# Kernel optimization log

Measured on AMD Instinct MI355X. Metric: run time of the kernel, lower is better.

The kernel has to match this reference:

```python
import jax, jax.numpy as jnp
import numpy as np

N_QUBITS = 4
DEPTH = 2
INV_SQRT2 = 0.7071067811865476

# --- batched real-valued 4-qubit state-vector simulator -------------------
# State: (N, 2, 2, 2, 2). All gates used (H, RY, CNOT) are real matrices, so
# the whole simulation runs in real float32 arithmetic.

def _apply_h(state, q):
    s = jnp.moveaxis(state, 1 + q, 1)
    a0, a1 = s[:, 0], s[:, 1]
    s = jnp.stack([(a0 + a1) * INV_SQRT2, (a0 - a1) * INV_SQRT2], axis=1)
    return jnp.moveaxis(s, 1, 1 + q)

def _apply_ry(state, theta, q):
    # theta: scalar (shared weight) or (N,) per-sample encoding angle
    s = jnp.moveaxis(state, 1 + q, 1)
    a0, a1 = s[:, 0], s[:, 1]
    theta = jnp.asarray(theta)
    c = jnp.cos(theta * 0.5)
    sn = jnp.sin(theta * 0.5)
    if c.ndim:  # per-sample angles -> broadcast over remaining qubit axes
        c = c.reshape(c.shape[0], *([1] * (a0.ndim - 1)))
        sn = sn.reshape(sn.shape[0], *([1] * (a0.ndim - 1)))
    s = jnp.stack([c * a0 - sn * a1, sn * a0 + c * a1], axis=1)
    return jnp.moveaxis(s, 1, 1 + q)

def _apply_cnot(state, c, t):
    s = jnp.moveaxis(state, (1 + c, 1 + t), (1, 2))
    s = jnp.concatenate([s[:, :1], s[:, 1:, ::-1]], axis=1)
    return jnp.moveaxis(s, (1, 2), (1 + c, 1 + t))

def _expval_z(state, q):
    p = jnp.moveaxis(state, 1 + q, 1) ** 2
    p = p.reshape(p.shape[0], 2, -1).sum(-1)
    return p[:, 0] - p[:, 1]

def _run_circuit(angles, weights):
    # angles: (N, 4); weights: (DEPTH, 2*N_QUBITS)
    N = angles.shape[0]
    state = jnp.zeros((N, 2, 2, 2, 2), dtype=angles.dtype).at[:, 0, 0, 0, 0].set(1.0)
    # encoding: H + RY(feature) per qubit
    for q in range(N_QUBITS):
        state = _apply_h(state, q)
        state = _apply_ry(state, angles[:, q], q)
    # pure_single_circuit: per depth, RY layer -> CNOT chain -> RY layer
    for d in range(DEPTH):
        for q in range(N_QUBITS):
            state = _apply_ry(state, weights[d, q], q)
        for q in range(N_QUBITS - 1):
            state = _apply_cnot(state, q, q + 1)
        for q in range(N_QUBITS):
            state = _apply_ry(state, weights[d, N_QUBITS + q], q)
    return jnp.stack([_expval_z(state, q) for q in range(N_QUBITS)], axis=1)  # (N, 4)


def setup_inputs() -> dict:
    key = jax.random.key(0)
    k1, k2 = jax.random.split(key)
    x = jax.random.uniform(k1, (4096, 1, 28, 28), dtype=jnp.float32)
    # TorchLayer default init: uniform in [0, 2*pi)
    weights = jax.random.uniform(k2, (DEPTH, 2 * N_QUBITS), dtype=jnp.float32) * (2.0 * np.pi)
    return {"x": x, "weights": weights, "kernel_size": 2}


def reference(x, weights, kernel_size):
    B, C, H, W = x.shape  # C == 1
    k = kernel_size  # 2
    # Extract non-overlapping 2x2 patches in the same (i, j) loop order as the
    # original: rows outer, cols inner, row-major flatten within each patch.
    p = x.reshape(B, H // k, k, W // k, k)
    p = p.transpose(0, 1, 3, 2, 4).reshape(B, -1, k * k)  # (B, P, 4)
    P = p.shape[1]
    angles = p.reshape(B * P, k * k)
    ev = _run_circuit(angles, weights)            # (B*P, 4)
    return ev.reshape(B, P * N_QUBITS)            # concat over patches on dim 1
```

## Files before the change

### kernel.cpp

```cpp
#include <hip/hip_runtime.h>


constexpr float INV_SQRT2f = 0.7071067811865476f;

#define TOTAL_CIRCUITS (4096 * 196)

__global__ __launch_bounds__(256) void quanv_kernel(
    const float* __restrict__ x,
    const float* __restrict__ w,
    float* __restrict__ out)
{
    __shared__ float tw[20];
    const int tid = threadIdx.x;
    if (tid < 12) {
        const int q = tid & 3;
        if (tid < 8) {
            const float half_ang = (tid < 4) ? 0.5f * (w[4 + q] + w[8 + q])
                                             : 0.5f * w[12 + q];
            float s, c;
            __sincosf(half_ang, &s, &c);
            const int base = (tid < 4) ? 0 : 8;
            tw[base + q]     = c;
            tw[base + 4 + q] = s;
        } else {
            tw[16 + q] = w[q];
        }
    }
    __syncthreads();

    const int t = blockIdx.x * 256 + tid;
    const int b  = t / 196;
    const int p  = t - b * 196;
    const int pi = p / 14;
    const int pj = p - pi * 14;

    const float* xp = x + b * 784 + pi * 56 + pj * 2;
    const float2 r0 = *reinterpret_cast<const float2*>(xp);
    const float2 r1 = *reinterpret_cast<const float2*>(xp + 28);
    const float ang[4] = { r0.x, r0.y, r1.x, r1.y };

    float v0[4], v1[4];
    #pragma unroll
    for (int q = 0; q < 4; ++q) {
        float s, c;
        __sincosf(0.5f * (ang[q] + tw[16 + q]), &s, &c);
        v0[q] = (c - s) * INV_SQRT2f;
        v1[q] = (c + s) * INV_SQRT2f;
    }

    float psi[16];
    {
        float p01[4];
        p01[0] = v0[0] * v0[1]; p01[1] = v0[0] * v1[1];
        p01[2] = v1[0] * v0[1]; p01[3] = v1[0] * v1[1];
        float p012[8];
        #pragma unroll
        for (int i = 0; i < 4; ++i) {
            p012[2 * i]     = p01[i] * v0[2];
            p012[2 * i + 1] = p01[i] * v1[2];
        }
        #pragma unroll
        for (int i = 0; i < 8; ++i) {
            psi[2 * i]     = p012[i] * v0[3];
            psi[2 * i + 1] = p012[i] * v1[3];
        }
    }

#define CNOT_GATE(C, T)                                                        \
    {                                                                          \
        const int bc = 1 << (3 - (C)), bt = 1 << (3 - (T));                    \
        _Pragma("unroll")                                                      \
        for (int i = 0; i < 16; ++i)                                           \
            if ((i & bc) && !(i & bt)) {                                       \
                const float tmp = psi[i];                                      \
                psi[i] = psi[i | bt];                                          \
                psi[i | bt] = tmp;                                             \
            }                                                                  \
    }

#define RY_GATE(Q, CC, SS)                                                     \
    {                                                                          \
        const int bq = 1 << (3 - (Q));                                         \
        _Pragma("unroll")                                                      \
        for (int i = 0; i < 16; ++i)                                           \
            if (!(i & bq)) {                                                   \
                const float a0 = psi[i], a1 = psi[i | bq];                     \
                psi[i]      = (CC) * a0 - (SS) * a1;                           \
                psi[i | bq] = (SS) * a0 + (CC) * a1;                           \
            }                                                                  \
    }

    CNOT_GATE(0, 1); CNOT_GATE(1, 2); CNOT_GATE(2, 3);

    #pragma unroll
    for (int q = 0; q < 4; ++q) {
        const float c = tw[q], s = tw[4 + q];
        RY_GATE(q, c, s);
    }

    CNOT_GATE(0, 1); CNOT_GATE(1, 2); CNOT_GATE(2, 3);

    #pragma unroll
    for (int q = 0; q < 4; ++q) {
        const float c = tw[8 + q], s = tw[12 + q];
        RY_GATE(q, c, s);
    }

    float sq[16];
    #pragma unroll
    for (int i = 0; i < 16; ++i) sq[i] = psi[i] * psi[i];

    float ev[4];
    #pragma unroll
    for (int q = 0; q < 4; ++q) {
        const int bq = 1 << (3 - q);
        float pos = 0.0f, neg = 0.0f;
        #pragma unroll
        for (int i = 0; i < 16; ++i) {
            if (i & bq) neg += sq[i];
            else        pos += sq[i];
        }
        ev[q] = pos - neg;
    }

    float4 o;
    o.x = ev[0]; o.y = ev[1]; o.z = ev[2]; o.w = ev[3];
    *reinterpret_cast<float4*>(out + 4 * t) = o;
}

extern "C" void kernel_launch(void* const* d_in, const int* in_sizes, int n_in,
                              void* d_out, int out_size, void* d_ws, size_t ws_size,
                              hipStream_t stream) {
    const float* x = (const float*)d_in[0];
    const float* w = (const float*)d_in[1];
    float* out = (float*)d_out;
    (void)in_sizes; (void)n_in; (void)d_ws; (void)ws_size; (void)out_size;

    const int total = TOTAL_CIRCUITS;
    const int block = 256;
    const int grid = total / block;
    quanv_kernel<<<grid, block, 0, stream>>>(x, w, out);
}
```

Baseline: 73.37 us.

## Fold final RY layer into analytic Z expectation and compute weight trig per thread

Removes the last RY layer from the state simulation. The Z expectation for each qubit is instead computed analytically as cos(theta)*<Z> - sin(theta)*2*Re<psi0|psi1>, using sums and cross-products of the pre-rotation amplitudes. Weight sin/cos values are now computed redundantly in every thread in registers, which drops the shared-memory table and the __syncthreads. This trades shared-memory traffic and a barrier for a few extra transcendental calls per thread.

```diff
diff --git a/kernel.cpp b/kernel.cpp
--- a/kernel.cpp
+++ b/kernel.cpp
@@ -10,25 +10,19 @@
     const float* __restrict__ w,
     float* __restrict__ out)
 {
-    __shared__ float tw[20];
-    const int tid = threadIdx.x;
-    if (tid < 12) {
-        const int q = tid & 3;
-        if (tid < 8) {
-            const float half_ang = (tid < 4) ? 0.5f * (w[4 + q] + w[8 + q])
-                                             : 0.5f * w[12 + q];
-            float s, c;
-            __sincosf(half_ang, &s, &c);
-            const int base = (tid < 4) ? 0 : 8;
-            tw[base + q]     = c;
-            tw[base + 4 + q] = s;
-        } else {
-            tw[16 + q] = w[q];
-        }
+    float w0[4], c2[4], s2[4], c3[4], s3d[4];
+    #pragma unroll
+    for (int q = 0; q < 4; ++q) {
+        w0[q] = w[q];
+        const float h2 = 0.5f * (w[4 + q] + w[8 + q]);
+        __sincosf(h2, &s2[q], &c2[q]);
+        float sf, cf;
+        __sincosf(w[12 + q], &sf, &cf);
+        c3[q]  = cf;
+        s3d[q] = 2.0f * sf;
     }
-    __syncthreads();
 
-    const int t = blockIdx.x * 256 + tid;
+    const int t = blockIdx.x * 256 + threadIdx.x;
     const int b  = t / 196;
     const int p  = t - b * 196;
     const int pi = p / 14;
@@ -43,7 +37,7 @@
     #pragma unroll
     for (int q = 0; q < 4; ++q) {
         float s, c;
-        __sincosf(0.5f * (ang[q] + tw[16 + q]), &s, &c);
+        __sincosf(0.5f * (ang[q] + w0[q]), &s, &c);
         v0[q] = (c - s) * INV_SQRT2f;
         v1[q] = (c + s) * INV_SQRT2f;
     }
@@ -93,38 +87,41 @@
     CNOT_GATE(0, 1); CNOT_GATE(1, 2); CNOT_GATE(2, 3);
 
     #pragma unroll
-    for (int q = 0; q < 4; ++q) {
-        const float c = tw[q], s = tw[4 + q];
-        RY_GATE(q, c, s);
-    }
+    for (int q = 0; q < 4; ++q) RY_GATE(q, c2[q], s2[q]);
 
     CNOT_GATE(0, 1); CNOT_GATE(1, 2); CNOT_GATE(2, 3);
-
-    #pragma unroll
-    for (int q = 0; q < 4; ++q) {
-        const float c = tw[8 + q], s = tw[12 + q];
-        RY_GATE(q, c, s);
-    }
 
     float sq[16];
     #pragma unroll
     for (int i = 0; i < 16; ++i) sq[i] = psi[i] * psi[i];
 
-    float ev[4];
+    float A[8], B[8];
     #pragma unroll
-    for (int q = 0; q < 4; ++q) {
-        const int bq = 1 << (3 - q);
-        float pos = 0.0f, neg = 0.0f;
-        #pragma unroll
-        for (int i = 0; i < 16; ++i) {
-            if (i & bq) neg += sq[i];
-            else        pos += sq[i];
-        }
-        ev[q] = pos - neg;
-    }
+    for (int m = 0; m < 8; ++m) { A[m] = sq[m] + sq[m + 8]; B[m] = sq[m] - sq[m + 8]; }
+    const float D0 = ((B[0] + B[1]) + (B[2] + B[3])) + ((B[4] + B[5]) + (B[6] + B[7]));
+    float G[4], H[4];
+    #pragma unroll
+    for (int k = 0; k < 4; ++k) { G[k] = A[k] + A[k + 4]; H[k] = A[k] - A[k + 4]; }
+    const float D1 = (H[0] + H[1]) + (H[2] + H[3]);
+    const float D2 = (G[0] + G[1]) - (G[2] + G[3]);
+    const float D3 = (G[0] + G[2]) - (G[1] + G[3]);
+
+    float C0 = 0.f, C1 = 0.f, C2 = 0.f, C3 = 0.f;
+    #pragma unroll
+    for (int i = 0; i < 8; ++i)  C0 += psi[i] * psi[i + 8];
+    #pragma unroll
+    for (int i = 0; i < 16; ++i) if (!(i & 4)) C1 += psi[i] * psi[i | 4];
+    #pragma unroll
+    for (int i = 0; i < 16; ++i) if (!(i & 2)) C2 += psi[i] * psi[i | 2];
+    #pragma unroll
+    for (int i = 0; i < 16; ++i) if (!(i & 1)) C3 += psi[i] * psi[i | 1];
 
     float4 o;
-    o.x = ev[0]; o.y = ev[1]; o.z = ev[2]; o.w = ev[3];
+    o.x = c3[0] * D0 - s3d[0] * C0;
+    o.y = c3[1] * D1 - s3d[1] * C1;
+    o.z = c3[2] * D2 - s3d[2] * C2;
+    o.w = c3[3] * D3 - s3d[3] * C3;
+
     *reinterpret_cast<float4*>(out + 4 * t) = o;
 }
 
@@ -136,8 +133,5 @@
     float* out = (float*)d_out;
     (void)in_sizes; (void)n_in; (void)d_ws; (void)ws_size; (void)out_size;
 
-    const int total = TOTAL_CIRCUITS;
-    const int block = 256;
-    const int grid = total / block;
-    quanv_kernel<<<grid, block, 0, stream>>>(x, w, out);
+    quanv_kernel<<<TOTAL_CIRCUITS / 256, 256, 0, stream>>>(x, w, out);
 }
```

New measurement: 73.45 us. No clear change (+0.1%).
